# Performance work log

Hardware: AMD Instinct MI355X
Metric: run time of the kernel (lower is better)

Reference implementation:

```python
import jax, jax.numpy as jnp
import numpy as np

B, CDD, HIS, T, L, D, K = 64, 5, 100, 30, 3, 256, 10
THRESHOLD = 0.1


def setup_inputs() -> dict:
    key = jax.random.key(0)
    k1, k2, k3, k4 = jax.random.split(key, 4)
    cdd_repr = jax.random.normal(k1, (B, CDD, D), dtype=jnp.float32)
    his_repr = jax.random.normal(k2, (B, HIS, D), dtype=jnp.float32)
    his_embedding = jax.random.normal(k3, (B, HIS, T, L, D), dtype=jnp.float32)
    # xavier_normal init for Linear(D, D)
    W_sel = jax.random.normal(k4, (D, D), dtype=jnp.float32) * np.sqrt(2.0 / (D + D))
    b_sel = jnp.zeros((D,), dtype=jnp.float32)
    return {"cdd_repr": cdd_repr, "his_repr": his_repr,
            "his_embedding": his_embedding, "W_sel": W_sel, "b_sel": b_sel}


def _l2_normalize(x, eps=1e-12):
    # matches torch F.normalize(dim=-1)
    n = jnp.linalg.norm(x, axis=-1, keepdims=True)
    return x / jnp.maximum(n, eps)


def reference(cdd_repr, his_repr, his_embedding, W_sel, b_sel):
    # selectionProject (Linear) + L2 normalize
    cdd_p = _l2_normalize(cdd_repr @ W_sel.T + b_sel)   # [B, CDD, D]
    his_p = _l2_normalize(his_repr @ W_sel.T + b_sel)   # [B, HIS, D]

    # news-level attention scores [B, CDD, HIS]
    attn = jnp.einsum('bcd,bhd->bch', cdd_p, his_p)

    # top-k over history
    attn_topk, idx = jax.lax.top_k(attn, K)             # [B, CDD, K]

    # multi-dim gather of history embeddings -> [B, CDD, K, T, L, D]
    his_activated = his_embedding[jnp.arange(B)[:, None, None], idx]

    # threshold masking: zero out weights below threshold, scale embeddings
    w = jnp.where(attn_topk < THRESHOLD, 0.0, attn_topk)
    his_activated = his_activated * w[:, :, :, None, None, None]

    return his_activated, idx
```

## Files before the change

### kernel.cpp

```cpp
#include <hip/hip_runtime.h>
#include <hip/hip_bf16.h>

#define NB   64
#define NCDD 5
#define NHIS 100
#define ND   256
#define NK   10
#define TLD  23040
#define THRESH 0.1f
#define NEG_INF (-3.402823466e38f)

typedef float f32x4 __attribute__((ext_vector_type(4)));

__global__ __launch_bounds__(256) void proj_norm_kernel(
    const float* __restrict__ X,
    const float* __restrict__ W,
    const float* __restrict__ bvec,
    float* __restrict__ Y)
{
    __shared__ float red[4][16];
    const int r0  = blockIdx.x * 16;
    const int tid = threadIdx.x;

    const float bias = bvec[tid];
    float acc[16];
#pragma unroll
    for (int r = 0; r < 16; ++r) acc[r] = bias;

    const float* wrow = W + (size_t)tid * ND;
    for (int k = 0; k < ND; k += 4) {
        const float4 w4 = *(const float4*)(wrow + k);
#pragma unroll
        for (int r = 0; r < 16; ++r) {
            const float4 x4 = *(const float4*)(X + (size_t)(r0 + r) * ND + k);
            acc[r] += w4.x * x4.x + w4.y * x4.y + w4.z * x4.z + w4.w * x4.w;
        }
    }

    const int wave = tid >> 6, lane = tid & 63;
#pragma unroll
    for (int r = 0; r < 16; ++r) {
        float v = acc[r] * acc[r];
        for (int off = 32; off; off >>= 1) v += __shfl_xor(v, off);
        if (lane == 0) red[wave][r] = v;
    }
    __syncthreads();

#pragma unroll
    for (int r = 0; r < 16; ++r) {
        const float s = red[0][r] + red[1][r] + red[2][r] + red[3][r];
        const float scale = 1.0f / fmaxf(sqrtf(s), 1e-12f);
        Y[(size_t)(r0 + r) * ND + tid] = acc[r] * scale;
    }
}

__global__ __launch_bounds__(256) void cdd_attn_topk_kernel(
    const float* __restrict__ cdd_repr,
    const float* __restrict__ W,
    const float* __restrict__ bvec,
    const float* __restrict__ his_p,
    float* __restrict__ out_idx_f,
    int* __restrict__ ws_idx,
    float* __restrict__ ws_w)
{
    __shared__ float cvec[ND];
    __shared__ float attn_s[NHIS];
    __shared__ float red[4];
    const int bc  = blockIdx.x;
    const int b   = bc / NCDD;
    const int tid = threadIdx.x;
    const int wave = tid >> 6, lane = tid & 63;

    float acc = bvec[tid];
    const float* wrow = W + (size_t)tid * ND;
    const float* xrow = cdd_repr + (size_t)bc * ND;
    for (int k = 0; k < ND; k += 4) {
        const float4 w4 = *(const float4*)(wrow + k);
        const float4 x4 = *(const float4*)(xrow + k);
        acc += w4.x * x4.x + w4.y * x4.y + w4.z * x4.z + w4.w * x4.w;
    }
    float ss = acc * acc;
    for (int off = 32; off; off >>= 1) ss += __shfl_xor(ss, off);
    if (lane == 0) red[wave] = ss;
    __syncthreads();
    const float s = red[0] + red[1] + red[2] + red[3];
    const float scale = 1.0f / fmaxf(sqrtf(s), 1e-12f);
    cvec[tid] = acc * scale;
    __syncthreads();

    const float4 c4 = ((const float4*)cvec)[lane];
    for (int h = wave; h < NHIS; h += 4) {
        const float4 h4 =
            ((const float4*)(his_p + ((size_t)b * NHIS + h) * ND))[lane];
        float v = c4.x * h4.x + c4.y * h4.y + c4.z * h4.z + c4.w * h4.w;
        for (int off = 32; off; off >>= 1) v += __shfl_xor(v, off);
        if (lane == 0) attn_s[h] = v;
    }
    __syncthreads();

    if (wave == 0) {
        float v0 = attn_s[lane];
        float v1 = (lane + 64 < NHIS) ? attn_s[lane + 64] : NEG_INF;
#pragma unroll
        for (int k = 0; k < NK; ++k) {
            float lv; int li;
            if (v1 > v0) { lv = v1; li = lane + 64; }
            else         { lv = v0; li = lane; }
            for (int off = 1; off < 64; off <<= 1) {
                const float ov = __shfl_xor(lv, off);
                const int   oi = __shfl_xor(li, off);
                if (ov > lv || (ov == lv && oi < li)) { lv = ov; li = oi; }
            }
            if (lane == 0) {
                const float w = (lv < THRESH) ? 0.0f : lv;
                const int g = bc * NK + k;
                ws_idx[g] = li;
                ws_w[g]   = w;
                out_idx_f[g] = (float)li;
            }
            if (li == lane)            v0 = NEG_INF;
            else if (li == lane + 64)  v1 = NEG_INF;
        }
    }
}

__global__ __launch_bounds__(256) void gather_kernel(
    const float* __restrict__ his_emb,
    const int* __restrict__ ws_idx,
    const float* __restrict__ ws_w,
    float* __restrict__ out)
{
    const int orig = blockIdx.x;
    const int g = (orig & 7) * 400 + (orig >> 3);
    const int b = g / (NCDD * NK);
    const int tid = threadIdx.x;
    const float w = ws_w[g];

    f32x4* __restrict__ dst = (f32x4*)(out + (size_t)g * TLD);

    if (w == 0.0f) {
        const f32x4 z = {0.f, 0.f, 0.f, 0.f};
#pragma unroll
        for (int it = 0; it < 22; ++it)
            __builtin_nontemporal_store(z, dst + tid + it * 256);
        if (tid < 128)
            __builtin_nontemporal_store(z, dst + 22 * 256 + tid);
        return;
    }

    const int idx = ws_idx[g];
    const f32x4* __restrict__ src =
        (const f32x4*)(his_emb + ((size_t)b * NHIS + idx) * TLD);

#pragma unroll 4
    for (int it = 0; it < 22; ++it) {
        const int i = tid + it * 256;
        f32x4 v = src[i];
        v *= w;
        __builtin_nontemporal_store(v, dst + i);
    }
    if (tid < 128) {
        const int i = 22 * 256 + tid;
        f32x4 v = src[i];
        v *= w;
        __builtin_nontemporal_store(v, dst + i);
    }
}

extern "C" void kernel_launch(void* const* d_in, const int* in_sizes, int n_in,
                              void* d_out, int out_size, void* d_ws, size_t ws_size,
                              hipStream_t stream)
{
    const float* cdd_repr = (const float*)d_in[0];
    const float* his_repr = (const float*)d_in[1];
    const float* his_emb  = (const float*)d_in[2];
    const float* W_sel    = (const float*)d_in[3];
    const float* b_sel    = (const float*)d_in[4];
    float* out = (float*)d_out;

    char* ws = (char*)d_ws;
    float* his_p = (float*)(ws);
    int*   idx_i = (int*)  (ws + 6553600);
    float* w_w   = (float*)(ws + 6566400);

    float* out_idx_f = out + (size_t)NB * NCDD * NK * TLD;

    proj_norm_kernel<<<(NB * NHIS) / 16, 256, 0, stream>>>(his_repr, W_sel, b_sel, his_p);
    cdd_attn_topk_kernel<<<NB * NCDD, 256, 0, stream>>>(cdd_repr, W_sel, b_sel,
                                                        his_p, out_idx_f, idx_i, w_w);
    gather_kernel<<<NB * NCDD * NK, 256, 0, stream>>>(his_emb, idx_i, w_w, out);
}
```

Before: 179.2 us.

## Batch cdd projection into his projection kernel and batch gather loads

Moves the candidate projection and normalisation out of the per-(b,c) attention kernel into the batched projection kernel, so the 320 attention blocks no longer each read the full weight matrix. The gather kernel now issues eight loads before their stores to raise memory-level parallelism. It also replaces the nontemporal stores with ordinary stores. That could change cache write behaviour on the large output stream.

```diff
diff --git a/kernel.cpp b/kernel.cpp
--- a/kernel.cpp
+++ b/kernel.cpp
@@ -9,18 +9,25 @@
 #define TLD  23040
 #define THRESH 0.1f
 #define NEG_INF (-3.402823466e38f)
+#define NROWS_HIS 6400
+#define NROWS_CDD 320
 
 typedef float f32x4 __attribute__((ext_vector_type(4)));
 
-__global__ __launch_bounds__(256) void proj_norm_kernel(
-    const float* __restrict__ X,
+__global__ __launch_bounds__(256) void proj_norm_all(
+    const float* __restrict__ his_repr,
+    const float* __restrict__ cdd_repr,
     const float* __restrict__ W,
     const float* __restrict__ bvec,
-    float* __restrict__ Y)
+    float* __restrict__ Yall)
 {
     __shared__ float red[4][16];
     const int r0  = blockIdx.x * 16;
     const int tid = threadIdx.x;
+
+    const float* __restrict__ X = (r0 < NROWS_HIS)
+        ? (his_repr + (size_t)r0 * ND)
+        : (cdd_repr + (size_t)(r0 - NROWS_HIS) * ND);
 
     const float bias = bvec[tid];
     float acc[16];
@@ -32,7 +39,7 @@
         const float4 w4 = *(const float4*)(wrow + k);
 #pragma unroll
         for (int r = 0; r < 16; ++r) {
-            const float4 x4 = *(const float4*)(X + (size_t)(r0 + r) * ND + k);
+            const float4 x4 = *(const float4*)(X + (size_t)r * ND + k);
             acc[r] += w4.x * x4.x + w4.y * x4.y + w4.z * x4.z + w4.w * x4.w;
         }
     }
@@ -50,14 +57,12 @@
     for (int r = 0; r < 16; ++r) {
         const float s = red[0][r] + red[1][r] + red[2][r] + red[3][r];
         const float scale = 1.0f / fmaxf(sqrtf(s), 1e-12f);
-        Y[(size_t)(r0 + r) * ND + tid] = acc[r] * scale;
+        Yall[(size_t)(r0 + r) * ND + tid] = acc[r] * scale;
     }
 }
 
-__global__ __launch_bounds__(256) void cdd_attn_topk_kernel(
-    const float* __restrict__ cdd_repr,
-    const float* __restrict__ W,
-    const float* __restrict__ bvec,
+__global__ __launch_bounds__(256) void attn_topk_kernel(
+    const float* __restrict__ cdd_p,
     const float* __restrict__ his_p,
     float* __restrict__ out_idx_f,
     int* __restrict__ ws_idx,
@@ -65,27 +70,12 @@
 {
     __shared__ float cvec[ND];
     __shared__ float attn_s[NHIS];
-    __shared__ float red[4];
     const int bc  = blockIdx.x;
     const int b   = bc / NCDD;
     const int tid = threadIdx.x;
     const int wave = tid >> 6, lane = tid & 63;
 
-    float acc = bvec[tid];
-    const float* wrow = W + (size_t)tid * ND;
-    const float* xrow = cdd_repr + (size_t)bc * ND;
-    for (int k = 0; k < ND; k += 4) {
-        const float4 w4 = *(const float4*)(wrow + k);
-        const float4 x4 = *(const float4*)(xrow + k);
-        acc += w4.x * x4.x + w4.y * x4.y + w4.z * x4.z + w4.w * x4.w;
-    }
-    float ss = acc * acc;
-    for (int off = 32; off; off >>= 1) ss += __shfl_xor(ss, off);
-    if (lane == 0) red[wave] = ss;
-    __syncthreads();
-    const float s = red[0] + red[1] + red[2] + red[3];
-    const float scale = 1.0f / fmaxf(sqrtf(s), 1e-12f);
-    cvec[tid] = acc * scale;
+    cvec[tid] = cdd_p[(size_t)bc * ND + tid];
     __syncthreads();
 
     const float4 c4 = ((const float4*)cvec)[lane];
@@ -141,10 +131,8 @@
     if (w == 0.0f) {
         const f32x4 z = {0.f, 0.f, 0.f, 0.f};
 #pragma unroll
-        for (int it = 0; it < 22; ++it)
-            __builtin_nontemporal_store(z, dst + tid + it * 256);
-        if (tid < 128)
-            __builtin_nontemporal_store(z, dst + 22 * 256 + tid);
+        for (int it = 0; it < 22; ++it) dst[tid + it * 256] = z;
+        if (tid < 128) dst[22 * 256 + tid] = z;
         return;
     }
 
@@ -152,18 +140,23 @@
     const f32x4* __restrict__ src =
         (const f32x4*)(his_emb + ((size_t)b * NHIS + idx) * TLD);
 
-#pragma unroll 4
-    for (int it = 0; it < 22; ++it) {
-        const int i = tid + it * 256;
-        f32x4 v = src[i];
-        v *= w;
-        __builtin_nontemporal_store(v, dst + i);
-    }
+    f32x4 v[8];
+#pragma unroll
+    for (int j = 0; j < 8; ++j) v[j] = src[tid + j * 256];
+#pragma unroll
+    for (int j = 0; j < 8; ++j) dst[tid + j * 256] = v[j] * w;
+#pragma unroll
+    for (int j = 0; j < 8; ++j) v[j] = src[tid + (8 + j) * 256];
+#pragma unroll
+    for (int j = 0; j < 8; ++j) dst[tid + (8 + j) * 256] = v[j] * w;
+#pragma unroll
+    for (int j = 0; j < 6; ++j) v[j] = src[tid + (16 + j) * 256];
+#pragma unroll
+    for (int j = 0; j < 6; ++j) dst[tid + (16 + j) * 256] = v[j] * w;
     if (tid < 128) {
         const int i = 22 * 256 + tid;
-        f32x4 v = src[i];
-        v *= w;
-        __builtin_nontemporal_store(v, dst + i);
+        f32x4 t = src[i];
+        dst[i] = t * w;
     }
 }
 
@@ -179,14 +172,17 @@
     float* out = (float*)d_out;
 
     char* ws = (char*)d_ws;
-    float* his_p = (float*)(ws);
-    int*   idx_i = (int*)  (ws + 6553600);
-    float* w_w   = (float*)(ws + 6566400);
+    float* Yall  = (float*)ws;
+    float* his_p = Yall;
+    float* cdd_p = Yall + (size_t)NROWS_HIS * ND;
+    int*   idx_i = (int*)  (ws + 6881280);
+    float* w_w   = (float*)(ws + 6894080);
 
     float* out_idx_f = out + (size_t)NB * NCDD * NK * TLD;
 
-    proj_norm_kernel<<<(NB * NHIS) / 16, 256, 0, stream>>>(his_repr, W_sel, b_sel, his_p);
-    cdd_attn_topk_kernel<<<NB * NCDD, 256, 0, stream>>>(cdd_repr, W_sel, b_sel,
-                                                        his_p, out_idx_f, idx_i, w_w);
+    proj_norm_all<<<(NROWS_HIS + NROWS_CDD) / 16, 256, 0, stream>>>(
+        his_repr, cdd_repr, W_sel, b_sel, Yall);
+    attn_topk_kernel<<<NB * NCDD, 256, 0, stream>>>(cdd_p, his_p,
+                                                    out_idx_f, idx_i, w_w);
     gather_kernel<<<NB * NCDD * NK, 256, 0, stream>>>(his_emb, idx_i, w_w, out);
 }
```

Measured after the change: 176.6 us. No clear change (-1.4%).
